# Kernel tuning notes

Hardware: AMD Instinct MI355X
Metric: run time of the kernel (lower is better)

The kernel has to match this reference:

```python
import jax, jax.numpy as jnp
import numpy as np

B, S, H, NH, HD = 1, 2048, 2048, 16, 128
ROPE_THETA = 10000.0


def _rope_tables():
    inv_freq = 1.0 / (ROPE_THETA ** (np.arange(0, HD, 2, dtype=np.float32) / HD))
    pos = np.arange(S, dtype=np.float32)
    freqs = pos[:, None] * inv_freq[None, :]          # [S, HD/2]
    emb = np.concatenate([freqs, freqs], axis=-1)     # [S, HD]
    cos = np.broadcast_to(np.cos(emb)[None], (B, S, HD)).copy()
    sin = np.broadcast_to(np.sin(emb)[None], (B, S, HD)).copy()
    return jnp.asarray(cos), jnp.asarray(sin)


def setup_inputs() -> dict:
    key = jax.random.key(0)
    ks = jax.random.split(key, 6)
    cos, sin = _rope_tables()
    scale = 0.02
    return {
        "query_states": jax.random.normal(ks[0], (B, S, H), jnp.float32),
        "key_states": jax.random.normal(ks[1], (B, S, H), jnp.float32),
        "cos": cos,
        "sin": sin,
        "Wq": jax.random.normal(ks[2], (H, NH * HD), jnp.float32).T * scale,
        "Wk": jax.random.normal(ks[3], (H, NH * HD), jnp.float32).T * scale,
        "Wv": jax.random.normal(ks[4], (H, NH * HD), jnp.float32).T * scale,
        "Wo": jax.random.normal(ks[5], (NH * HD, H), jnp.float32).T * scale,
    }


def _rotate_half(t):
    # Faithful to source: cat of halves WITHOUT negation (identity op).
    return jnp.concatenate([t[..., : HD // 2], t[..., HD // 2 :]], axis=-1)


def reference(query_states, key_states, cos, sin, Wq, Wk, Wv, Wo):
    def heads(x, W):
        # nn.Linear: x @ W.T ; then [B,S,NH,HD] -> [B,NH,S,HD]
        return (x @ W.T).reshape(B, S, NH, HD).transpose(0, 2, 1, 3)

    # NOTE: source swaps projections (k_proj on query, q_proj on key) - kept faithful.
    q = heads(query_states, Wk)
    k = heads(key_states, Wq)
    v = heads(key_states, Wv)

    c = cos[:, None]  # [B,1,S,HD]
    s = sin[:, None]
    q = q * c + _rotate_half(q) * s
    k = k * c + _rotate_half(k) * s

    scaling = HD ** -0.5
    scores = jnp.einsum("bhqd,bhkd->bhqk", q, k) * scaling
    attn_weights = jax.nn.softmax(scores.astype(jnp.float32), axis=-1).astype(q.dtype)
    attn = jnp.einsum("bhqk,bhkd->bhqd", attn_weights, v)
    attn = attn.transpose(0, 2, 1, 3).reshape(B, S, NH * HD)
    out = attn @ Wo.T
    return out, attn_weights
```

## Files before the change

### kernel.cpp

```cpp
#include <hip/hip_runtime.h>

#define SQ   2048
#define HD   128
#define NH   16
#define HDIM 2048

typedef short bf16x8 __attribute__((ext_vector_type(8)));
typedef float f32x4  __attribute__((ext_vector_type(4)));

__device__ __forceinline__ unsigned short f2bf(float x) {
    union { float f; unsigned u; } v; v.f = x;
    unsigned r = v.u + 0x7fffu + ((v.u >> 16) & 1u);
    return (unsigned short)(r >> 16);
}

__device__ __forceinline__ void gl_lds16(const void* g, void* l) {
    __builtin_amdgcn_global_load_lds(
        (const __attribute__((address_space(1))) unsigned*)g,
        (__attribute__((address_space(3))) unsigned*)l, 16, 0, 0);
}

template<int ROWS>
__device__ __forceinline__ void stage_tile(const unsigned short* __restrict__ src,
                                           long ld, unsigned short* dst)
{
    const int tid = threadIdx.x;
    #pragma unroll
    for (int c = 0; c < ROWS / 16; ++c) {
        int o   = c * 4096 + tid * 16;
        int row = o >> 8;
        int pch = (o >> 4) & 15;
        int lch = pch ^ (row & 7);
        gl_lds16(src + (long)row * ld + lch * 8, (char*)dst + o);
    }
}

__device__ __forceinline__ bf16x8 frag_ld(const unsigned short* buf, int row, int chunk)
{
    int o = row * 256 + ((chunk ^ (row & 7)) << 4);
    return *(const bf16x8*)((const char*)buf + o);
}

__device__ __forceinline__ void p_st(unsigned short* buf, int row, int col, unsigned short v)
{
    int o = row * 256 + ((((col >> 3) ^ (row & 7))) << 4) + ((col & 7) << 1);
    *(unsigned short*)((char*)buf + o) = v;
}

struct CvtPtrs {
    const float* s[6];
    unsigned short* d[6];
};

__global__ __launch_bounds__(256)
void k_cvt6(CvtPtrs p, long n)
{
    const float* __restrict__ s = p.s[blockIdx.z];
    unsigned short* __restrict__ d = p.d[blockIdx.z];
    long i = ((long)blockIdx.x * 256 + threadIdx.x) * 8;
    if (i >= n) return;
    float4 a = *(const float4*)(s + i);
    float4 b = *(const float4*)(s + i + 4);
    unsigned short t[8] = { f2bf(a.x), f2bf(a.y), f2bf(a.z), f2bf(a.w),
                            f2bf(b.x), f2bf(b.y), f2bf(b.z), f2bf(b.w) };
    *(int4*)(d + i) = *(const int4*)t;
}

template<int BM, int WM>
__device__ __forceinline__ void gemm_core(
    const unsigned short* Ap, const unsigned short* Bp,
    int K, int lda, int ldb,
    unsigned short* As, unsigned short* Bs,
    f32x4 (&acc)[WM][4])
{
    const int tid  = threadIdx.x;
    const int lane = tid & 63;
    const int w    = tid >> 6;
    const int wr   = w >> 1, wc = w & 1;
    const int l15  = lane & 15, lk = lane >> 4;

    for (int kt = 0; kt < K; kt += 32) {
        __syncthreads();
        #pragma unroll
        for (int c = 0; c < BM / 64; ++c) {
            int o = c * 4096 + tid * 16;
            int r = o >> 6, k0 = (o & 63) >> 1;
            gl_lds16(Ap + (long)r * lda + kt + k0, (char*)As + o);
        }
        #pragma unroll
        for (int c = 0; c < 2; ++c) {
            int o = c * 4096 + tid * 16;
            int r = o >> 6, k0 = (o & 63) >> 1;
            gl_lds16(Bp + (long)r * ldb + kt + k0, (char*)Bs + o);
        }
        __syncthreads();
        bf16x8 af[WM], bfr[4];
        #pragma unroll
        for (int m = 0; m < WM; ++m) {
            int arow = wr * (BM / 2) + m * 16 + l15;
            af[m] = *(const bf16x8*)((const char*)As + arow * 64 + lk * 16);
        }
        #pragma unroll
        for (int n = 0; n < 4; ++n) {
            int bcol = wc * 64 + n * 16 + l15;
            bfr[n] = *(const bf16x8*)((const char*)Bs + bcol * 64 + lk * 16);
        }
        #pragma unroll
        for (int m = 0; m < WM; ++m)
            #pragma unroll
            for (int n = 0; n < 4; ++n)
                acc[m][n] = __builtin_amdgcn_mfma_f32_16x16x32_bf16(
                    af[m], bfr[n], acc[m][n], 0, 0, 0);
    }
}

__global__ __launch_bounds__(256)
void k_proj(const unsigned short* __restrict__ XqB, const unsigned short* __restrict__ XkB,
            const unsigned short* __restrict__ WkB, const unsigned short* __restrict__ WqB,
            const unsigned short* __restrict__ WvB,
            const float* __restrict__ cosp, const float* __restrict__ sinp,
            unsigned short* __restrict__ Qp, unsigned short* __restrict__ Kp,
            unsigned short* __restrict__ Vp)
{
    __shared__ __align__(16) unsigned short As[128 * 32];
    __shared__ __align__(16) unsigned short Bs[128 * 32];

    const int lin = (blockIdx.z * 16 + blockIdx.y) * 16 + blockIdx.x;
    const int xcd = lin & 7, kk = lin >> 3;
    const int s   = xcd + (kk >> 4) * 8;
    const int w2  = kk & 15;
    const int blk = s * 16 + w2;
    const int z   = blk >> 8;
    const int r   = blk & 255;
    const int sid = r >> 4, wi = r & 15;
    const int row0 = ((sid >> 2) * 4 + (wi >> 2)) * 128;
    const int col0 = ((sid & 3) * 4 + (wi & 3)) * 128;

    const unsigned short* Ap = (z == 0 ? XqB : XkB) + (long)row0 * HDIM;
    const unsigned short* Bp = (z == 0 ? WkB : (z == 1 ? WqB : WvB)) + (long)col0 * HDIM;

    f32x4 acc[4][4];
    #pragma unroll
    for (int m = 0; m < 4; ++m)
        #pragma unroll
        for (int n = 0; n < 4; ++n) acc[m][n] = (f32x4){0.f, 0.f, 0.f, 0.f};

    gemm_core<128, 4>(Ap, Bp, HDIM, HDIM, HDIM, As, Bs, acc);

    const int tid = threadIdx.x, lane = tid & 63, w = tid >> 6;
    const int wr = w >> 1, wc = w & 1, l15 = lane & 15, lk = lane >> 4;

    if (z < 2) {
        unsigned short* dst = (z == 0) ? Qp : Kp;
        const float sc = (z == 0) ? 0.088388347648318447f : 1.0f;
        #pragma unroll
        for (int m = 0; m < 4; ++m)
            #pragma unroll
            for (int n = 0; n < 4; ++n)
                #pragma unroll
                for (int j = 0; j < 4; ++j) {
                    int grow = row0 + wr * 64 + m * 16 + lk * 4 + j;
                    int gcol = col0 + wc * 64 + n * 16 + l15;
                    int head = gcol >> 7, d = gcol & 127;
                    float cs = (cosp[(long)grow * HD + d] + sinp[(long)grow * HD + d]) * sc;
                    dst[(long)head * SQ * HD + (long)grow * HD + d] = f2bf(acc[m][n][j] * cs);
                }
    } else {
        #pragma unroll
        for (int m = 0; m < 4; ++m)
            #pragma unroll
            for (int n = 0; n < 4; ++n)
                #pragma unroll
                for (int j = 0; j < 4; ++j) {
                    int grow = row0 + wr * 64 + m * 16 + lk * 4 + j;
                    int gcol = col0 + wc * 64 + n * 16 + l15;
                    int head = gcol >> 7, d = gcol & 127;
                    Vp[(long)head * HD * SQ + (long)d * SQ + grow] = f2bf(acc[m][n][j]);
                }
    }
}

__global__ __launch_bounds__(256)
void k_attn(const unsigned short* __restrict__ Qp, const unsigned short* __restrict__ Kp,
            const unsigned short* __restrict__ Vp, float* __restrict__ attw,
            unsigned short* __restrict__ attnB)
{
    __shared__ __align__(16) unsigned short lds[40960];
    unsigned short* KV0 = lds;
    unsigned short* KV1 = lds + 16384;
    unsigned short* PQ  = lds + 32768;
    float* sred = (float*)PQ;

    const int lin = blockIdx.y * gridDim.x + blockIdx.x;
    const int wg  = (lin & 7) * 64 + (lin >> 3);
    const int z   = wg >> 5;
    const int r0  = (wg & 31) * 64;

    const unsigned short* Qh = Qp + (long)z * SQ * HD + (long)r0 * HD;
    const unsigned short* Kh = Kp + (long)z * SQ * HD;
    const unsigned short* Vh = Vp + (long)z * HD * SQ;
    float* Wout = attw + (long)z * SQ * SQ;

    const int tid = threadIdx.x, lane = tid & 63, w = tid >> 6;
    const int wr = w >> 1, wc = w & 1, l15 = lane & 15, lk = lane >> 4;

    stage_tile<64>(Qh, HD, PQ);
    stage_tile<128>(Kh, HD, KV0);
    __syncthreads();

    bf16x8 qf[2][4];
    #pragma unroll
    for (int m = 0; m < 2; ++m)
        #pragma unroll
        for (int s = 0; s < 4; ++s)
            qf[m][s] = frag_ld(PQ, wr * 32 + m * 16 + l15, 4 * s + lk);

    float lreg[8];
    #pragma unroll
    for (int r = 0; r < 8; ++r) lreg[r] = 0.0f;

    for (int t = 0; t < 16; ++t) {
        unsigned short* cur = (t & 1) ? KV1 : KV0;
        unsigned short* nxt = (t & 1) ? KV0 : KV1;
        if (t < 15) stage_tile<128>(Kh + (long)(t + 1) * 128 * HD, HD, nxt);
        f32x4 s_[2][4];
        #pragma unroll
        for (int m = 0; m < 2; ++m)
            #pragma unroll
            for (int n = 0; n < 4; ++n) s_[m][n] = (f32x4){0.f, 0.f, 0.f, 0.f};
        #pragma unroll
        for (int ks = 0; ks < 4; ++ks) {
            bf16x8 bf[4];
            #pragma unroll
            for (int n = 0; n < 4; ++n)
                bf[n] = frag_ld(cur, wc * 64 + n * 16 + l15, 4 * ks + lk);
            #pragma unroll
            for (int m = 0; m < 2; ++m)
                #pragma unroll
                for (int n = 0; n < 4; ++n)
                    s_[m][n] = __builtin_amdgcn_mfma_f32_16x16x32_bf16(
                        qf[m][ks], bf[n], s_[m][n], 0, 0, 0);
        }
        #pragma unroll
        for (int m = 0; m < 2; ++m)
            #pragma unroll
            for (int j = 0; j < 4; ++j)
                lreg[m * 4 + j] += __expf(s_[m][0][j]) + __expf(s_[m][1][j]) +
                                   __expf(s_[m][2][j]) + __expf(s_[m][3][j]);
        __syncthreads();
    }

    stage_tile<128>(Kh, HD, KV0);

    #pragma unroll
    for (int r = 0; r < 8; ++r)
        #pragma unroll
        for (int d = 1; d < 16; d <<= 1)
            lreg[r] += __shfl_xor(lreg[r], d, 64);
    if (l15 == 0) {
        #pragma unroll
        for (int r = 0; r < 8; ++r) {
            int lr = wr * 32 + (r >> 2) * 16 + lk * 4 + (r & 3);
            sred[wc * 64 + lr] = lreg[r];
        }
    }
    __syncthreads();
    if (tid < 64) sred[128 + tid] = 1.0f / (sred[tid] + sred[64 + tid]);
    __syncthreads();

    float lrow[8];
    #pragma unroll
    for (int m = 0; m < 2; ++m)
        #pragma unroll
        for (int j = 0; j < 4; ++j)
            lrow[m * 4 + j] = sred[128 + wr * 32 + m * 16 + lk * 4 + j];
    __syncthreads();

    f32x4 pv[2][4];
    #pragma unroll
    for (int m = 0; m < 2; ++m)
        #pragma unroll
        for (int n = 0; n < 4; ++n) pv[m][n] = (f32x4){0.f, 0.f, 0.f, 0.f};

    for (int t = 0; t < 16; ++t) {
        stage_tile<128>(Vh + (long)t * 128, SQ, KV1);
        f32x4 s_[2][4];
        #pragma unroll
        for (int m = 0; m < 2; ++m)
            #pragma unroll
            for (int n = 0; n < 4; ++n) s_[m][n] = (f32x4){0.f, 0.f, 0.f, 0.f};
        #pragma unroll
        for (int ks = 0; ks < 4; ++ks) {
            bf16x8 bf[4];
            #pragma unroll
            for (int n = 0; n < 4; ++n)
                bf[n] = frag_ld(KV0, wc * 64 + n * 16 + l15, 4 * ks + lk);
            #pragma unroll
            for (int m = 0; m < 2; ++m)
                #pragma unroll
                for (int n = 0; n < 4; ++n)
                    s_[m][n] = __builtin_amdgcn_mfma_f32_16x16x32_bf16(
                        qf[m][ks], bf[n], s_[m][n], 0, 0, 0);
        }
        #pragma unroll
        for (int m = 0; m < 2; ++m)
            #pragma unroll
            for (int n = 0; n < 4; ++n)
                #pragma unroll
                for (int j = 0; j < 4; ++j) {
                    const int r   = m * 4 + j;
                    const int lr  = wr * 32 + m * 16 + lk * 4 + j;
                    const int col = wc * 64 + n * 16 + l15;
                    s_[m][n][j] = __expf(s_[m][n][j]) * lrow[r];
                    p_st(PQ, lr, col, f2bf(s_[m][n][j]));
                }
        __syncthreads();
        if (t < 15) stage_tile<128>(Kh + (long)(t + 1) * 128 * HD, HD, KV0);
        #pragma unroll
        for (int m = 0; m < 2; ++m)
            #pragma unroll
            for (int n = 0; n < 4; ++n)
                #pragma unroll
                for (int j = 0; j < 4; ++j) {
                    const int lr  = wr * 32 + m * 16 + lk * 4 + j;
                    const int col = wc * 64 + n * 16 + l15;
                    __builtin_nontemporal_store(
                        s_[m][n][j], &Wout[(long)(r0 + lr) * SQ + t * 128 + col]);
                }
        #pragma unroll
        for (int ks = 0; ks < 4; ++ks) {
            bf16x8 pa[2], vb[4];
            #pragma unroll
            for (int m = 0; m < 2; ++m)
                pa[m] = frag_ld(PQ, wr * 32 + m * 16 + l15, 4 * ks + lk);
            #pragma unroll
            for (int n = 0; n < 4; ++n)
                vb[n] = frag_ld(KV1, wc * 64 + n * 16 + l15, 4 * ks + lk);
            #pragma unroll
            for (int m = 0; m < 2; ++m)
                #pragma unroll
                for (int n = 0; n < 4; ++n)
                    pv[m][n] = __builtin_amdgcn_mfma_f32_16x16x32_bf16(
                        pa[m], vb[n], pv[m][n], 0, 0, 0);
        }
        __syncthreads();
    }

    #pragma unroll
    for (int m = 0; m < 2; ++m)
        #pragma unroll
        for (int n = 0; n < 4; ++n)
            #pragma unroll
            for (int j = 0; j < 4; ++j) {
                long grow = r0 + wr * 32 + m * 16 + lk * 4 + j;
                int  gcol = wc * 64 + n * 16 + l15;
                attnB[grow * HDIM + (long)z * HD + gcol] = f2bf(pv[m][n][j]);
            }
}

__global__ __launch_bounds__(256)
void k_out(const unsigned short* __restrict__ attnB, const unsigned short* __restrict__ WoB,
           float* __restrict__ out)
{
    __shared__ __align__(16) unsigned short As[64 * 32];
    __shared__ __align__(16) unsigned short Bs[128 * 32];

    const int lin = blockIdx.y * gridDim.x + blockIdx.x;
    const int xcd = lin & 7, kk = lin >> 3;
    const int s   = xcd + (kk >> 5) * 8;
    const int wi  = kk & 31;
    const int row0 = ((s >> 2) * 8 + (wi >> 2)) * 64;
    const int col0 = ((s & 3) * 4 + (wi & 3)) * 128;

    const unsigned short* Ap = attnB + (long)row0 * HDIM;
    const unsigned short* Bp = WoB + (long)col0 * HDIM;

    f32x4 acc[2][4];
    #pragma unroll
    for (int m = 0; m < 2; ++m)
        #pragma unroll
        for (int n = 0; n < 4; ++n) acc[m][n] = (f32x4){0.f, 0.f, 0.f, 0.f};

    gemm_core<64, 2>(Ap, Bp, HDIM, HDIM, HDIM, As, Bs, acc);

    const int tid = threadIdx.x, lane = tid & 63, w = tid >> 6;
    const int wr = w >> 1, wc = w & 1, l15 = lane & 15, lk = lane >> 4;
    #pragma unroll
    for (int m = 0; m < 2; ++m)
        #pragma unroll
        for (int n = 0; n < 4; ++n)
            #pragma unroll
            for (int j = 0; j < 4; ++j) {
                long grow = row0 + wr * 32 + m * 16 + lk * 4 + j;
                long gcol = col0 + wc * 64 + n * 16 + l15;
                out[grow * HDIM + gcol] = acc[m][n][j];
            }
}

extern "C" void kernel_launch(void* const* d_in, const int* in_sizes, int n_in,
                              void* d_out, int out_size, void* d_ws, size_t ws_size,
                              hipStream_t stream)
{
    const float* Xq   = (const float*)d_in[0];
    const float* Xk   = (const float*)d_in[1];
    const float* cosp = (const float*)d_in[2];
    const float* sinp = (const float*)d_in[3];
    const float* Wq   = (const float*)d_in[4];
    const float* Wk   = (const float*)d_in[5];
    const float* Wv   = (const float*)d_in[6];
    const float* Wo   = (const float*)d_in[7];

    float* out  = (float*)d_out;
    float* attw = out + (long)SQ * HDIM;

    const long TE = (long)SQ * HDIM;

    unsigned short* Qp    = (unsigned short*)d_ws;
    unsigned short* Kp    = Qp + TE;
    unsigned short* Vp    = Kp + TE;
    unsigned short* attnB = Vp + TE;
    unsigned short* WoB   = attnB + TE;

    unsigned short* stg = (unsigned short*)attw;
    unsigned short* XqB = stg;
    unsigned short* XkB = stg + TE;
    unsigned short* WkB = stg + 2 * TE;
    unsigned short* WqB = stg + 3 * TE;
    unsigned short* WvB = stg + 4 * TE;

    dim3 blk(256);

    CvtPtrs cp;
    cp.s[0] = Xq; cp.d[0] = XqB;
    cp.s[1] = Xk; cp.d[1] = XkB;
    cp.s[2] = Wk; cp.d[2] = WkB;
    cp.s[3] = Wq; cp.d[3] = WqB;
    cp.s[4] = Wv; cp.d[4] = WvB;
    cp.s[5] = Wo; cp.d[5] = WoB;
    k_cvt6<<<dim3((int)(TE / (8 * 256)), 1, 6), blk, 0, stream>>>(cp, TE);

    k_proj<<<dim3(16, 16, 3), blk, 0, stream>>>(XqB, XkB, WkB, WqB, WvB,
                                                cosp, sinp, Qp, Kp, Vp);

    k_attn<<<dim3(32, 16), blk, 0, stream>>>(Qp, Kp, Vp, attw, attnB);

    k_out<<<dim3(16, 32), blk, 0, stream>>>(attnB, WoB, out);
}
```

Before: 234.3 us.

## Use exp2 with folded log2e, vectorize attn-weight stores from LDS, add setprio

Folds log2(e) into the Q scaling so softmax exponentials use the native exp2 instruction instead of __expf. The attention-weight output is no longer written as scattered scalar stores from MFMA fragments. It is read back row-wise from the bf16 P tile in LDS (with the XOR swizzle) and written as coalesced 16-byte nontemporal stores. MFMA sections are wrapped in s_setprio to favour matrix issue. The stored weights are now bf16-rounded values rather than full fp32, which slightly changes output precision.

New measurement: 244.5 us. +4.4%, slower.

```diff
diff --git a/kernel.cpp b/kernel.cpp
--- a/kernel.cpp
+++ b/kernel.cpp
@@ -8,10 +8,21 @@
 typedef short bf16x8 __attribute__((ext_vector_type(8)));
 typedef float f32x4  __attribute__((ext_vector_type(4)));
 
+#if __has_builtin(__builtin_amdgcn_exp2f)
+#define EXP2(x) __builtin_amdgcn_exp2f(x)
+#else
+#define EXP2(x) exp2f(x)
+#endif
+
 __device__ __forceinline__ unsigned short f2bf(float x) {
     union { float f; unsigned u; } v; v.f = x;
     unsigned r = v.u + 0x7fffu + ((v.u >> 16) & 1u);
     return (unsigned short)(r >> 16);
+}
+
+__device__ __forceinline__ float bf2f(unsigned short u) {
+    union { unsigned u32; float f; } v; v.u32 = (unsigned)u << 16;
+    return v.f;
 }
 
 __device__ __forceinline__ void gl_lds16(const void* g, void* l) {
@@ -152,7 +163,8 @@
 
     if (z < 2) {
         unsigned short* dst = (z == 0) ? Qp : Kp;
-        const float sc = (z == 0) ? 0.088388347648318447f : 1.0f;
+        const float sc = (z == 0) ? (0.088388347648318447f * 1.4426950408889634f)
+                                  : 1.0f;
         #pragma unroll
         for (int m = 0; m < 4; ++m)
             #pragma unroll
@@ -228,6 +240,7 @@
         for (int m = 0; m < 2; ++m)
             #pragma unroll
             for (int n = 0; n < 4; ++n) s_[m][n] = (f32x4){0.f, 0.f, 0.f, 0.f};
+        __builtin_amdgcn_s_setprio(1);
         #pragma unroll
         for (int ks = 0; ks < 4; ++ks) {
             bf16x8 bf[4];
@@ -241,12 +254,13 @@
                     s_[m][n] = __builtin_amdgcn_mfma_f32_16x16x32_bf16(
                         qf[m][ks], bf[n], s_[m][n], 0, 0, 0);
         }
+        __builtin_amdgcn_s_setprio(0);
         #pragma unroll
         for (int m = 0; m < 2; ++m)
             #pragma unroll
             for (int j = 0; j < 4; ++j)
-                lreg[m * 4 + j] += __expf(s_[m][0][j]) + __expf(s_[m][1][j]) +
-                                   __expf(s_[m][2][j]) + __expf(s_[m][3][j]);
+                lreg[m * 4 + j] += EXP2(s_[m][0][j]) + EXP2(s_[m][1][j]) +
+                                   EXP2(s_[m][2][j]) + EXP2(s_[m][3][j]);
         __syncthreads();
     }
 
@@ -289,6 +303,7 @@
         for (int m = 0; m < 2; ++m)
             #pragma unroll
             for (int n = 0; n < 4; ++n) s_[m][n] = (f32x4){0.f, 0.f, 0.f, 0.f};
+        __builtin_amdgcn_s_setprio(1);
         #pragma unroll
         for (int ks = 0; ks < 4; ++ks) {
             bf16x8 bf[4];
@@ -302,6 +317,7 @@
                     s_[m][n] = __builtin_amdgcn_mfma_f32_16x16x32_bf16(
                         qf[m][ks], bf[n], s_[m][n], 0, 0, 0);
         }
+        __builtin_amdgcn_s_setprio(0);
         #pragma unroll
         for (int m = 0; m < 2; ++m)
             #pragma unroll
@@ -311,22 +327,26 @@
                     const int r   = m * 4 + j;
                     const int lr  = wr * 32 + m * 16 + lk * 4 + j;
                     const int col = wc * 64 + n * 16 + l15;
-                    s_[m][n][j] = __expf(s_[m][n][j]) * lrow[r];
-                    p_st(PQ, lr, col, f2bf(s_[m][n][j]));
+                    p_st(PQ, lr, col, f2bf(EXP2(s_[m][n][j]) * lrow[r]));
                 }
         __syncthreads();
         if (t < 15) stage_tile<128>(Kh + (long)(t + 1) * 128 * HD, HD, KV0);
         #pragma unroll
-        for (int m = 0; m < 2; ++m)
-            #pragma unroll
-            for (int n = 0; n < 4; ++n)
-                #pragma unroll
-                for (int j = 0; j < 4; ++j) {
-                    const int lr  = wr * 32 + m * 16 + lk * 4 + j;
-                    const int col = wc * 64 + n * 16 + l15;
-                    __builtin_nontemporal_store(
-                        s_[m][n][j], &Wout[(long)(r0 + lr) * SQ + t * 128 + col]);
-                }
+        for (int rb = 0; rb < 4; ++rb) {
+            const int row = rb * 16 + (tid >> 4);
+            const int ch  = tid & 15;
+            bf16x8 pr = *(const bf16x8*)((const char*)PQ + row * 256 +
+                                         ((ch ^ (row & 7)) << 4));
+            f32x4 lo, hi;
+            lo[0] = bf2f((unsigned short)pr[0]); lo[1] = bf2f((unsigned short)pr[1]);
+            lo[2] = bf2f((unsigned short)pr[2]); lo[3] = bf2f((unsigned short)pr[3]);
+            hi[0] = bf2f((unsigned short)pr[4]); hi[1] = bf2f((unsigned short)pr[5]);
+            hi[2] = bf2f((unsigned short)pr[6]); hi[3] = bf2f((unsigned short)pr[7]);
+            float* dst = &Wout[(long)(r0 + row) * SQ + t * 128 + ch * 8];
+            __builtin_nontemporal_store(lo, (f32x4*)dst);
+            __builtin_nontemporal_store(hi, (f32x4*)(dst + 4));
+        }
+        __builtin_amdgcn_s_setprio(1);
         #pragma unroll
         for (int ks = 0; ks < 4; ++ks) {
             bf16x8 pa[2], vb[4];
@@ -343,6 +363,7 @@
                     pv[m][n] = __builtin_amdgcn_mfma_f32_16x16x32_bf16(
                         pa[m], vb[n], pv[m][n], 0, 0, 0);
         }
+        __builtin_amdgcn_s_setprio(0);
         __syncthreads();
     }
 
```
